# Performance work log

Hardware: AMD Instinct MI355X
Metric: run time of the kernel (lower is better)

Reference implementation:

```python
import jax, jax.numpy as jnp
import numpy as np

B = 256          # batch
T = 256          # block_size (tril mask requires seq_len == 256)
E = 384          # n_embed
H = 6            # n_head
HS = E // H      # head_size = 64
EPS = 1e-5       # torch LayerNorm default


def layernorm(x, g, b):
    m = x.mean(-1, keepdims=True)
    v = x.var(-1, keepdims=True)  # population variance, matches torch LN
    return (x - m) * jax.lax.rsqrt(v + EPS) * g + b


def setup_inputs() -> dict:
    key = jax.random.key(0)
    ks = jax.random.split(key, 8)
    s = lambda i, shape: jax.random.normal(ks[i], shape, jnp.float32) * 0.02
    return {
        "x": jax.random.normal(ks[0], (B, T, E), jnp.float32),
        # per-head Q/K/V linears (bias=False) packed along output dim: [E, H*HS]
        "Wq": s(1, (E, E)), "Wk": s(2, (E, E)), "Wv": s(3, (E, E)),
        "Wo": s(4, (E, E)), "bo": jnp.zeros((E,), jnp.float32),
        "W1": s(5, (E, 4 * E)), "b1": jnp.zeros((4 * E,), jnp.float32),
        "W2": s(6, (4 * E, E)), "b2": jnp.zeros((E,), jnp.float32),
        "g1": jnp.ones((E,), jnp.float32), "be1": jnp.zeros((E,), jnp.float32),
        "g2": jnp.ones((E,), jnp.float32), "be2": jnp.zeros((E,), jnp.float32),
    }


def reference(x, Wq, Wk, Wv, Wo, bo, W1, b1, W2, b2, g1, be1, g2, be2):
    # Block.forward: ffwd(ln2(sa(ln1(x)) + x)) + x   (dropout = identity at eval)
    h = layernorm(x, g1, be1)                                  # [B,T,E]
    q = (h @ Wq).reshape(B, T, H, HS)
    k = (h @ Wk).reshape(B, T, H, HS)
    v = (h @ Wv).reshape(B, T, H, HS)
    wei = jnp.einsum('bqhd,bkhd->bhqk', q, k) * (HS ** -0.5)   # [B,H,T,T]
    mask = jnp.tril(jnp.ones((T, T), dtype=bool))
    wei = jnp.where(mask, wei, -jnp.inf)
    wei = jax.nn.softmax(wei, axis=-1)
    attn = jnp.einsum('bhqk,bkhd->bqhd', wei, v).reshape(B, T, E)
    sa = attn @ Wo + bo                                        # output projection
    y = sa + x                                                 # residual 1
    h2 = layernorm(y, g2, be2)
    ff = jax.nn.relu(h2 @ W1 + b1) @ W2 + b2                   # FFN
    return ff + x                                              # residual 2 (to x!)
```

## Files before the change

### kernel.cpp

```cpp
#include <hip/hip_runtime.h>
#include <hip/hip_bf16.h>

typedef unsigned short bfu;
typedef __attribute__((ext_vector_type(8))) short short8;
typedef __attribute__((ext_vector_type(4))) float f32x4;

__device__ __forceinline__ bfu f2bf(float f) {
  return __builtin_bit_cast(bfu, __float2bfloat16(f));
}

__device__ __forceinline__ void gld16(const void* g, void* l) {
  __builtin_amdgcn_global_load_lds(
      (const __attribute__((address_space(1))) void*)g,
      (__attribute__((address_space(3))) void*)l, 16, 0, 0);
}

__device__ __forceinline__ int swz(int row, int slot) {
  const int unit = row >> 1;
  const int s8 = ((row & 1) << 2) | slot;
  return (unit << 7) + (((s8 ^ unit) & 7) << 4) + ((s8 >> 3) << 7);
}
__device__ __forceinline__ void unswz(int p, int& row, int& colel) {
  const int unit = p >> 7;
  const int s8 = ((p >> 4) & 7) ^ (unit & 7);
  row = (unit << 1) | (s8 >> 2);
  colel = (s8 & 3) << 3;
}

__global__ void transpose_w(const float* __restrict__ W, bfu* __restrict__ WT,
                            int K, int N) {
  int idx = blockIdx.x * 256 + threadIdx.x;
  if (idx >= K * N) return;
  int k = idx / N, n = idx - k * N;
  WT[(size_t)n * K + k] = f2bf(W[idx]);
}

__launch_bounds__(256)
__global__ void ln_kernel(const float* __restrict__ in, const float* __restrict__ g,
                          const float* __restrict__ be, bfu* __restrict__ out) {
  const int wv = threadIdx.x >> 6, ln = threadIdx.x & 63;
  const size_t row = (size_t)blockIdx.x * 4 + wv;
  const float* p = in + row * 384;
  float v[6], s = 0.f, ss = 0.f;
#pragma unroll
  for (int i = 0; i < 6; i++) { v[i] = p[i * 64 + ln]; s += v[i]; ss += v[i] * v[i]; }
#pragma unroll
  for (int m = 1; m < 64; m <<= 1) { s += __shfl_xor(s, m); ss += __shfl_xor(ss, m); }
  const float mean = s * (1.f / 384.f);
  const float rs = rsqrtf(ss * (1.f / 384.f) - mean * mean + 1e-5f);
  bfu* q = out + row * 384;
#pragma unroll
  for (int i = 0; i < 6; i++) {
    const int c = i * 64 + ln;
    q[c] = f2bf((v[i] - mean) * rs * g[c] + be[c]);
  }
}

template <int BIAS, int RELU, int OUTBF>
__launch_bounds__(256)
__global__ void gemm_kernel(const bfu* __restrict__ A, const bfu* __restrict__ Bt,
                            const float* __restrict__ bias,
                            void* __restrict__ Cout, int N, int K, int ntn) {
  __shared__ bfu a_sm[3][128 * 32];
  __shared__ bfu b_sm[3][128 * 32];
  const int tid = threadIdx.x;
  const int wv = tid >> 6, ln = tid & 63;
  const int cpx = gridDim.x >> 3;
  const int wg = (blockIdx.x & 7) * cpx + (blockIdx.x >> 3);
  const int bm = wg / ntn, bn = wg - bm * ntn;
  const int m0 = bm << 7, n0 = bn << 7;
  const int wr = wv >> 1, wc = wv & 1;
  const int fr = ln & 15, fslot = ln >> 4;

  f32x4 acc[4][4];
#pragma unroll
  for (int i = 0; i < 4; i++)
#pragma unroll
    for (int j = 0; j < 4; j++) acc[i][j] = f32x4{0.f, 0.f, 0.f, 0.f};

  auto stage = [&](int buf, int kt) {
#pragma unroll
    for (int i = 0; i < 2; ++i) {
      const int c = wv * 2 + i;
      const int p = c * 1024 + (ln << 4);
      int r, colel;
      unswz(p, r, colel);
      const int col = kt * 32 + colel;
      gld16(A  + (size_t)(m0 + r) * K + col, (char*)a_sm[buf] + c * 1024);
      gld16(Bt + (size_t)(n0 + r) * K + col, (char*)b_sm[buf] + c * 1024);
    }
  };

  const int nk = K >> 5;
  stage(0, 0);
  if (nk > 1) stage(1, 1);

  int cb = 0;
  for (int kt = 0; kt < nk; ++kt) {
    if (kt + 1 < nk) asm volatile("s_waitcnt vmcnt(4)" ::: "memory");
    else             asm volatile("s_waitcnt vmcnt(0)" ::: "memory");
    __builtin_amdgcn_s_barrier();
    __builtin_amdgcn_sched_barrier(0);
    if (kt + 2 < nk) {
      int sb = cb + 2; if (sb >= 3) sb -= 3;
      stage(sb, kt + 2);
    }
    short8 af[4], bfr[4];
#pragma unroll
    for (int mi = 0; mi < 4; mi++)
      af[mi] = *(const short8*)((const char*)a_sm[cb] + swz(wr * 64 + mi * 16 + fr, fslot));
#pragma unroll
    for (int ni = 0; ni < 4; ni++)
      bfr[ni] = *(const short8*)((const char*)b_sm[cb] + swz(wc * 64 + ni * 16 + fr, fslot));
#pragma unroll
    for (int mi = 0; mi < 4; mi++)
#pragma unroll
      for (int ni = 0; ni < 4; ni++)
        acc[mi][ni] = __builtin_amdgcn_mfma_f32_16x16x32_bf16(af[mi], bfr[ni], acc[mi][ni], 0, 0, 0);
    cb = (cb + 1 == 3) ? 0 : cb + 1;
  }

#pragma unroll
  for (int mi = 0; mi < 4; mi++) {
#pragma unroll
    for (int ni = 0; ni < 4; ni++) {
      const int row = m0 + wr * 64 + mi * 16 + ((ln >> 4) << 2);
      const int col = n0 + wc * 64 + ni * 16 + fr;
      float bv = 0.f;
      if (BIAS) bv = bias[col];
#pragma unroll
      for (int r = 0; r < 4; r++) {
        float v = acc[mi][ni][r] + bv;
        if (RELU) v = fmaxf(v, 0.f);
        const size_t idx = (size_t)(row + r) * N + col;
        if (OUTBF) ((bfu*)Cout)[idx] = f2bf(v);
        else       ((float*)Cout)[idx] = v;
      }
    }
  }
}

template <int LN>
__launch_bounds__(512)
__global__ void row_gemm(const bfu* __restrict__ A, const bfu* __restrict__ Bt,
                         const float* __restrict__ bias, const float* __restrict__ res,
                         const float* __restrict__ g, const float* __restrict__ be,
                         void* __restrict__ Cout, int K) {
  __shared__ bfu a_sm[4][128 * 32];
  __shared__ bfu b_sm[4][384 * 32];
  __shared__ float lnp[4][128][2];
  const int tid = threadIdx.x;
  const int wv = tid >> 6, ln = tid & 63;
  const int wr = wv >> 2, wc = wv & 3;
  const int fr = ln & 15, fslot = ln >> 4;
  const int m0 = blockIdx.x << 7;

  f32x4 acc[4][6];
#pragma unroll
  for (int i = 0; i < 4; i++)
#pragma unroll
    for (int j = 0; j < 6; j++) acc[i][j] = f32x4{0.f, 0.f, 0.f, 0.f};

  auto stage = [&](int buf, int kt) {
#pragma unroll
    for (int i = 0; i < 4; ++i) {
      const int c = wv * 4 + i;
      const int cc = (c < 8) ? c : (c - 8);
      const int p = cc * 1024 + (ln << 4);
      int r, colel;
      unswz(p, r, colel);
      const int col = kt * 32 + colel;
      if (c < 8)
        gld16(A + (size_t)(m0 + r) * K + col, (char*)a_sm[buf] + cc * 1024);
      else
        gld16(Bt + (size_t)r * K + col, (char*)b_sm[buf] + cc * 1024);
    }
  };

  const int nk = K >> 5;
#pragma unroll
  for (int i = 0; i < 3; ++i)
    if (i < nk) stage(i, i);

  for (int kt = 0; kt < nk; ++kt) {
    const int rem = nk - 1 - kt;
    if (rem >= 2)      asm volatile("s_waitcnt vmcnt(8)" ::: "memory");
    else if (rem == 1) asm volatile("s_waitcnt vmcnt(4)" ::: "memory");
    else               asm volatile("s_waitcnt vmcnt(0)" ::: "memory");
    __builtin_amdgcn_s_barrier();
    __builtin_amdgcn_sched_barrier(0);
    if (kt + 3 < nk) stage((kt + 3) & 3, kt + 3);
    const int cb = kt & 3;
    short8 af[4], bfr[6];
#pragma unroll
    for (int mi = 0; mi < 4; mi++)
      af[mi] = *(const short8*)((const char*)a_sm[cb] + swz(wr * 64 + mi * 16 + fr, fslot));
#pragma unroll
    for (int ni = 0; ni < 6; ni++)
      bfr[ni] = *(const short8*)((const char*)b_sm[cb] + swz(wc * 96 + ni * 16 + fr, fslot));
#pragma unroll
    for (int mi = 0; mi < 4; mi++)
#pragma unroll
      for (int ni = 0; ni < 6; ni++)
        acc[mi][ni] = __builtin_amdgcn_mfma_f32_16x16x32_bf16(af[mi], bfr[ni], acc[mi][ni], 0, 0, 0);
  }

  const int rq = (ln >> 4) << 2;
#pragma unroll
  for (int mi = 0; mi < 4; mi++) {
    const int row = wr * 64 + mi * 16 + rq;
#pragma unroll
    for (int ni = 0; ni < 6; ni++) {
      const int col = wc * 96 + ni * 16 + fr;
      const float bv = bias[col];
#pragma unroll
      for (int r = 0; r < 4; r++)
        acc[mi][ni][r] += bv + res[(size_t)(m0 + row + r) * 384 + col];
    }
  }

  if (LN) {
#pragma unroll
    for (int mi = 0; mi < 4; mi++) {
      float s[4] = {0.f, 0.f, 0.f, 0.f}, ss[4] = {0.f, 0.f, 0.f, 0.f};
#pragma unroll
      for (int ni = 0; ni < 6; ni++)
#pragma unroll
        for (int r = 0; r < 4; r++) {
          const float v = acc[mi][ni][r];
          s[r] += v; ss[r] += v * v;
        }
#pragma unroll
      for (int m = 1; m < 16; m <<= 1)
#pragma unroll
        for (int r = 0; r < 4; r++) {
          s[r] += __shfl_xor(s[r], m);
          ss[r] += __shfl_xor(ss[r], m);
        }
      if (fr == 0) {
#pragma unroll
        for (int r = 0; r < 4; r++) {
          lnp[wc][wr * 64 + mi * 16 + rq + r][0] = s[r];
          lnp[wc][wr * 64 + mi * 16 + rq + r][1] = ss[r];
        }
      }
    }
    __syncthreads();
#pragma unroll
    for (int mi = 0; mi < 4; mi++) {
#pragma unroll
      for (int r = 0; r < 4; r++) {
        const int row = wr * 64 + mi * 16 + rq + r;
        const float sm = lnp[0][row][0] + lnp[1][row][0] + lnp[2][row][0] + lnp[3][row][0];
        const float sq = lnp[0][row][1] + lnp[1][row][1] + lnp[2][row][1] + lnp[3][row][1];
        const float mean = sm * (1.f / 384.f);
        const float rs = rsqrtf(sq * (1.f / 384.f) - mean * mean + 1e-5f);
#pragma unroll
        for (int ni = 0; ni < 6; ni++) {
          const int col = wc * 96 + ni * 16 + fr;
          ((bfu*)Cout)[(size_t)(m0 + row) * 384 + col] =
              f2bf((acc[mi][ni][r] - mean) * rs * g[col] + be[col]);
        }
      }
    }
  } else {
#pragma unroll
    for (int mi = 0; mi < 4; mi++) {
      const int row = wr * 64 + mi * 16 + rq;
#pragma unroll
      for (int ni = 0; ni < 6; ni++) {
        const int col = wc * 96 + ni * 16 + fr;
#pragma unroll
        for (int r = 0; r < 4; r++)
          ((float*)Cout)[(size_t)(m0 + row + r) * 384 + col] = acc[mi][ni][r];
      }
    }
  }
}

#define KPAD 72
#define VPAD 264
#define PPAD 264

__launch_bounds__(512)
__global__ void attn_kernel(const bfu* __restrict__ qkv, bfu* __restrict__ ob) {
  __shared__ bfu k_sm[256 * KPAD];
  __shared__ bfu vt_sm[64 * VPAD];
  __shared__ bfu p_sm[8 * 16 * PPAD];
  const int b = blockIdx.x / 6, h = blockIdx.x - b * 6;
  const int tid = threadIdx.x;
  const int wv = tid >> 6, ln = tid & 63;
  const int fr = ln & 15, fc = (ln >> 4) << 3;
  const size_t inbase = (size_t)b * 256 * 1152 + h * 64;
  const bfu* qb = qkv + inbase;
  const bfu* kb = qkv + inbase + 384;
  const bfu* vb = qkv + inbase + 768;
  const size_t obase = (size_t)b * 256 * 384 + h * 64;

  {
    const int row = tid >> 1;
    const int dh = (tid & 1) << 5;
    const bfu* kg = kb + (size_t)row * 1152 + dh;
    const bfu* vg = vb + (size_t)row * 1152 + dh;
#pragma unroll
    for (int i = 0; i < 4; i++) {
      short8 t8 = *(const short8*)(kg + i * 8);
      *(short8*)&k_sm[row * KPAD + dh + i * 8] = t8;
      short8 v8 = *(const short8*)(vg + i * 8);
#pragma unroll
      for (int j = 0; j < 8; j++)
        vt_sm[(dh + i * 8 + j) * VPAD + row] = (bfu)v8[j];
    }
  }
  __syncthreads();

  bfu* pw = &p_sm[wv * 16 * PPAD];
  const int rq = (ln >> 4) << 2;

#pragma unroll
  for (int si = 0; si < 2; ++si) {
    const int s = si ? (15 - wv) : wv;
    const int qr0 = s << 4;
    const int nf = s + 1;
    short8 aq[2];
#pragma unroll
    for (int dc = 0; dc < 2; dc++)
      aq[dc] = *(const short8*)(qb + (size_t)(qr0 + fr) * 1152 + dc * 32 + fc);

    f32x4 sacc[16];
#pragma unroll
    for (int f = 0; f < 16; f++) sacc[f] = f32x4{0.f, 0.f, 0.f, 0.f};
#pragma unroll
    for (int f = 0; f < 16; f++) if (f < nf) {
#pragma unroll
      for (int dc = 0; dc < 2; dc++) {
        short8 kf = *(const short8*)&k_sm[(f * 16 + fr) * KPAD + dc * 32 + fc];
        sacc[f] = __builtin_amdgcn_mfma_f32_16x16x32_bf16(aq[dc], kf, sacc[f], 0, 0, 0);
      }
    }
    float mr[4] = {-3e38f, -3e38f, -3e38f, -3e38f};
#pragma unroll
    for (int f = 0; f < 16; f++) if (f < nf) {
#pragma unroll
      for (int r = 0; r < 4; r++) {
        float sv = sacc[f][r] * 0.125f;
        if (f * 16 + fr > qr0 + rq + r) sv = -3e38f;
        sacc[f][r] = sv;
        mr[r] = fmaxf(mr[r], sv);
      }
    }
#pragma unroll
    for (int msk = 1; msk < 16; msk <<= 1) {
#pragma unroll
      for (int r = 0; r < 4; r++) mr[r] = fmaxf(mr[r], __shfl_xor(mr[r], msk));
    }
    float ls[4] = {0.f, 0.f, 0.f, 0.f};
#pragma unroll
    for (int f = 0; f < 16; f++) if (f < nf) {
#pragma unroll
      for (int r = 0; r < 4; r++) {
        float p = __expf(sacc[f][r] - mr[r]);
        sacc[f][r] = p;
        ls[r] += p;
      }
    }
#pragma unroll
    for (int msk = 1; msk < 16; msk <<= 1) {
#pragma unroll
      for (int r = 0; r < 4; r++) ls[r] += __shfl_xor(ls[r], msk);
    }
#pragma unroll
    for (int f = 0; f < 16; f++) if (f < nf) {
#pragma unroll
      for (int r = 0; r < 4; r++)
        pw[(rq + r) * PPAD + f * 16 + fr] = f2bf(sacc[f][r]);
    }
    if (nf & 1) {
#pragma unroll
      for (int r = 0; r < 4; r++) pw[(rq + r) * PPAD + nf * 16 + fr] = 0;
    }
    f32x4 oc[4];
#pragma unroll
    for (int n = 0; n < 4; n++) oc[n] = f32x4{0.f, 0.f, 0.f, 0.f};
    const int kcs = (nf + 1) >> 1;
#pragma unroll
    for (int kc = 0; kc < 8; ++kc) if (kc < kcs) {
      short8 pa = *(const short8*)&pw[fr * PPAD + kc * 32 + fc];
#pragma unroll
      for (int n = 0; n < 4; n++) {
        short8 vf = *(const short8*)&vt_sm[(n * 16 + fr) * VPAD + kc * 32 + fc];
        oc[n] = __builtin_amdgcn_mfma_f32_16x16x32_bf16(pa, vf, oc[n], 0, 0, 0);
      }
    }
    float inv[4];
#pragma unroll
    for (int r = 0; r < 4; r++) inv[r] = 1.f / ls[r];
#pragma unroll
    for (int n = 0; n < 4; n++) {
#pragma unroll
      for (int r = 0; r < 4; r++)
        ob[obase + (size_t)(qr0 + rq + r) * 384 + n * 16 + fr] = f2bf(oc[n][r] * inv[r]);
    }
  }
}

extern "C" void kernel_launch(void* const* d_in, const int* in_sizes, int n_in,
                              void* d_out, int out_size, void* d_ws, size_t ws_size,
                              hipStream_t stream) {
  const float* x   = (const float*)d_in[0];
  const float* Wq  = (const float*)d_in[1];
  const float* Wk  = (const float*)d_in[2];
  const float* Wv  = (const float*)d_in[3];
  const float* Wo  = (const float*)d_in[4];
  const float* bo  = (const float*)d_in[5];
  const float* W1  = (const float*)d_in[6];
  const float* b1  = (const float*)d_in[7];
  const float* W2  = (const float*)d_in[8];
  const float* b2  = (const float*)d_in[9];
  const float* g1  = (const float*)d_in[10];
  const float* be1 = (const float*)d_in[11];
  const float* g2  = (const float*)d_in[12];
  const float* be2 = (const float*)d_in[13];
  float* out = (float*)d_out;
  char* ws = (char*)d_ws;

  bfu* wqkvT = (bfu*)(ws + 0);
  bfu* woT   = (bfu*)(ws + 884736);
  bfu* w1T   = (bfu*)(ws + 1179648);
  bfu* w2T   = (bfu*)(ws + 2359296);
  char* H    = ws + 3538944;
  char* BIG  = H + 50331648;
  bfu* hb    = (bfu*)BIG;
  bfu* qkvb  = (bfu*)(BIG + 50331648);
  bfu* attnb = (bfu*)BIG;
  bfu* h2b   = (bfu*)H;
  bfu* ab    = (bfu*)BIG;

  transpose_w<<<576, 256, 0, stream>>>(Wq, wqkvT, 384, 384);
  transpose_w<<<576, 256, 0, stream>>>(Wk, wqkvT + 384 * 384, 384, 384);
  transpose_w<<<576, 256, 0, stream>>>(Wv, wqkvT + 2 * 384 * 384, 384, 384);
  transpose_w<<<576, 256, 0, stream>>>(Wo, woT, 384, 384);
  transpose_w<<<2304, 256, 0, stream>>>(W1, w1T, 384, 1536);
  transpose_w<<<2304, 256, 0, stream>>>(W2, w2T, 1536, 384);

  ln_kernel<<<16384, 256, 0, stream>>>(x, g1, be1, hb);

  gemm_kernel<0, 0, 1><<<4608, 256, 0, stream>>>(hb, wqkvT, nullptr, qkvb, 1152, 384, 9);

  attn_kernel<<<1536, 512, 0, stream>>>(qkvb, attnb);

  row_gemm<1><<<512, 512, 0, stream>>>(attnb, woT, bo, x, g2, be2, h2b, 384);

  gemm_kernel<1, 1, 1><<<6144, 256, 0, stream>>>(h2b, w1T, b1, ab, 1536, 384, 12);

  row_gemm<0><<<512, 512, 0, stream>>>(ab, w2T, b2, x, nullptr, nullptr, out, 1536);
}
```

Measured before the change: 522.1 us.

## Replace GEMM with 8-wave 256x128 BK=64 pipelined kernel and fuse weight transposes

Introduces gemm8p, an 8-wave kernel with 256x128 tiles and K=64 stages in triple-buffered LDS, using a new row-XOR swizzle, split half-K MFMA phases, barriers and s_setprio around MFMA bursts. It is used for the QKV, FFN1 and FFN2 GEMMs, with FFN2 now adding the residual in a plain epilogue instead of row_gemm. The six weight transpose launches are merged into one kernel, and setprio is added to row_gemm. The aims are more operand reuse per tile, fewer barriers per K step and fewer launches, at the cost of much larger LDS use (about 144KB) that limits occupancy.

```diff
diff --git a/kernel.cpp b/kernel.cpp
--- a/kernel.cpp
+++ b/kernel.cpp
@@ -13,6 +13,10 @@
   __builtin_amdgcn_global_load_lds(
       (const __attribute__((address_space(1))) void*)g,
       (__attribute__((address_space(3))) void*)l, 16, 0, 0);
+}
+
+__device__ __forceinline__ int swz8(int row, int sl) {
+  return (row << 7) + (((sl ^ (row & 7)) & 7) << 4);
 }
 
 __device__ __forceinline__ int swz(int row, int slot) {
@@ -27,12 +31,27 @@
   colel = (s8 & 3) << 3;
 }
 
-__global__ void transpose_w(const float* __restrict__ W, bfu* __restrict__ WT,
-                            int K, int N) {
+__global__ void transpose_all(const float* __restrict__ Wq, const float* __restrict__ Wk,
+                              const float* __restrict__ Wv, const float* __restrict__ Wo,
+                              const float* __restrict__ W1, const float* __restrict__ W2,
+                              bfu* __restrict__ wqkvT, bfu* __restrict__ woT,
+                              bfu* __restrict__ w1T, bfu* __restrict__ w2T) {
   int idx = blockIdx.x * 256 + threadIdx.x;
-  if (idx >= K * N) return;
-  int k = idx / N, n = idx - k * N;
-  WT[(size_t)n * K + k] = f2bf(W[idx]);
+  if (idx < 4 * 147456) {
+    int r = idx / 147456, i = idx - r * 147456;
+    int k = i / 384, n = i - k * 384;
+    const float* W = r == 0 ? Wq : r == 1 ? Wk : r == 2 ? Wv : Wo;
+    bfu* dst = r < 3 ? wqkvT + r * 147456 : woT;
+    dst[n * 384 + k] = f2bf(W[i]);
+  } else if (idx < 4 * 147456 + 589824) {
+    int i = idx - 4 * 147456;
+    int k = i / 1536, n = i - k * 1536;
+    w1T[n * 384 + k] = f2bf(W1[i]);
+  } else if (idx < 4 * 147456 + 2 * 589824) {
+    int i = idx - 4 * 147456 - 589824;
+    int k = i / 384, n = i - k * 384;
+    w2T[(size_t)n * 1536 + k] = f2bf(W2[i]);
+  }
 }
 
 __launch_bounds__(256)
@@ -56,19 +75,18 @@
   }
 }
 
-template <int BIAS, int RELU, int OUTBF>
-__launch_bounds__(256)
-__global__ void gemm_kernel(const bfu* __restrict__ A, const bfu* __restrict__ Bt,
-                            const float* __restrict__ bias,
-                            void* __restrict__ Cout, int N, int K, int ntn) {
-  __shared__ bfu a_sm[3][128 * 32];
-  __shared__ bfu b_sm[3][128 * 32];
+template <int BIAS, int RELU, int RES, int OUTBF>
+__launch_bounds__(512)
+__global__ void gemm8p(const bfu* __restrict__ A, const bfu* __restrict__ Bt,
+                       const float* __restrict__ bias, const float* __restrict__ res,
+                       void* __restrict__ Cout, int N, int K, int ntn) {
+  __shared__ bfu sm[3][384 * 64];
   const int tid = threadIdx.x;
   const int wv = tid >> 6, ln = tid & 63;
   const int cpx = gridDim.x >> 3;
   const int wg = (blockIdx.x & 7) * cpx + (blockIdx.x >> 3);
   const int bm = wg / ntn, bn = wg - bm * ntn;
-  const int m0 = bm << 7, n0 = bn << 7;
+  const int m0 = bm << 8, n0 = bn << 7;
   const int wr = wv >> 1, wc = wv & 1;
   const int fr = ln & 15, fslot = ln >> 4;
 
@@ -78,53 +96,85 @@
 #pragma unroll
     for (int j = 0; j < 4; j++) acc[i][j] = f32x4{0.f, 0.f, 0.f, 0.f};
 
-  auto stage = [&](int buf, int kt) {
+  const int lr = ln >> 3;
+  const int lslot = (ln & 7) ^ lr;
+
+  auto stage = [&](int s, int kt) {
+    char* smA = (char*)sm[s];
+    char* smB = smA + 256 * 64 * 2;
+    const int kcol = (kt << 6) + (lslot << 3);
+#pragma unroll
+    for (int i = 0; i < 4; ++i) {
+      const int c = (wv << 2) + i;
+      gld16(A + (size_t)(m0 + (c << 3) + lr) * K + kcol, smA + (c << 10));
+    }
 #pragma unroll
     for (int i = 0; i < 2; ++i) {
-      const int c = wv * 2 + i;
-      const int p = c * 1024 + (ln << 4);
-      int r, colel;
-      unswz(p, r, colel);
-      const int col = kt * 32 + colel;
-      gld16(A  + (size_t)(m0 + r) * K + col, (char*)a_sm[buf] + c * 1024);
-      gld16(Bt + (size_t)(n0 + r) * K + col, (char*)b_sm[buf] + c * 1024);
+      const int c = (wv << 1) + i;
+      gld16(Bt + (size_t)(n0 + (c << 3) + lr) * K + kcol, smB + (c << 10));
     }
   };
 
-  const int nk = K >> 5;
+  const int nk = K >> 6;
   stage(0, 0);
-  if (nk > 1) stage(1, 1);
-
-  int cb = 0;
+  if (nk > 1) {
+    stage(1, 1);
+    asm volatile("s_waitcnt vmcnt(6)" ::: "memory");
+  } else {
+    asm volatile("s_waitcnt vmcnt(0)" ::: "memory");
+  }
+  __builtin_amdgcn_s_barrier();
+
   for (int kt = 0; kt < nk; ++kt) {
-    if (kt + 1 < nk) asm volatile("s_waitcnt vmcnt(4)" ::: "memory");
-    else             asm volatile("s_waitcnt vmcnt(0)" ::: "memory");
+    const int s = kt - (kt / 3) * 3;
+    const char* smA = (const char*)sm[s];
+    const char* smB = smA + 256 * 64 * 2;
+    if (kt + 2 < nk) stage((kt + 2) - ((kt + 2) / 3) * 3, kt + 2);
+    short8 af[4], bf[4];
+#pragma unroll
+    for (int mi = 0; mi < 4; mi++)
+      af[mi] = *(const short8*)(smA + swz8(wr * 64 + mi * 16 + fr, fslot));
+#pragma unroll
+    for (int ni = 0; ni < 4; ni++)
+      bf[ni] = *(const short8*)(smB + swz8(wc * 64 + ni * 16 + fr, fslot));
     __builtin_amdgcn_s_barrier();
+    asm volatile("s_waitcnt lgkmcnt(0)" ::: "memory");
     __builtin_amdgcn_sched_barrier(0);
-    if (kt + 2 < nk) {
-      int sb = cb + 2; if (sb >= 3) sb -= 3;
-      stage(sb, kt + 2);
-    }
-    short8 af[4], bfr[4];
+    __builtin_amdgcn_s_setprio(1);
 #pragma unroll
     for (int mi = 0; mi < 4; mi++)
-      af[mi] = *(const short8*)((const char*)a_sm[cb] + swz(wr * 64 + mi * 16 + fr, fslot));
+#pragma unroll
+      for (int ni = 0; ni < 4; ni++)
+        acc[mi][ni] = __builtin_amdgcn_mfma_f32_16x16x32_bf16(af[mi], bf[ni], acc[mi][ni], 0, 0, 0);
+    __builtin_amdgcn_s_setprio(0);
+    __builtin_amdgcn_s_barrier();
+#pragma unroll
+    for (int mi = 0; mi < 4; mi++)
+      af[mi] = *(const short8*)(smA + swz8(wr * 64 + mi * 16 + fr, 4 + fslot));
 #pragma unroll
     for (int ni = 0; ni < 4; ni++)
-      bfr[ni] = *(const short8*)((const char*)b_sm[cb] + swz(wc * 64 + ni * 16 + fr, fslot));
+      bf[ni] = *(const short8*)(smB + swz8(wc * 64 + ni * 16 + fr, 4 + fslot));
+    __builtin_amdgcn_s_barrier();
+    asm volatile("s_waitcnt lgkmcnt(0)" ::: "memory");
+    __builtin_amdgcn_sched_barrier(0);
+    __builtin_amdgcn_s_setprio(1);
 #pragma unroll
     for (int mi = 0; mi < 4; mi++)
 #pragma unroll
       for (int ni = 0; ni < 4; ni++)
-        acc[mi][ni] = __builtin_amdgcn_mfma_f32_16x16x32_bf16(af[mi], bfr[ni], acc[mi][ni], 0, 0, 0);
-    cb = (cb + 1 == 3) ? 0 : cb + 1;
-  }
-
+        acc[mi][ni] = __builtin_amdgcn_mfma_f32_16x16x32_bf16(af[mi], bf[ni], acc[mi][ni], 0, 0, 0);
+    __builtin_amdgcn_s_setprio(0);
+    if (kt + 2 < nk)      asm volatile("s_waitcnt vmcnt(6)" ::: "memory");
+    else if (kt + 1 < nk) asm volatile("s_waitcnt vmcnt(0)" ::: "memory");
+    __builtin_amdgcn_s_barrier();
+  }
+
+  const int rq = (ln >> 4) << 2;
 #pragma unroll
   for (int mi = 0; mi < 4; mi++) {
 #pragma unroll
     for (int ni = 0; ni < 4; ni++) {
-      const int row = m0 + wr * 64 + mi * 16 + ((ln >> 4) << 2);
+      const int row = m0 + wr * 64 + mi * 16 + rq;
       const int col = n0 + wc * 64 + ni * 16 + fr;
       float bv = 0.f;
       if (BIAS) bv = bias[col];
@@ -133,6 +183,7 @@
         float v = acc[mi][ni][r] + bv;
         if (RELU) v = fmaxf(v, 0.f);
         const size_t idx = (size_t)(row + r) * N + col;
+        if (RES) v += res[idx];
         if (OUTBF) ((bfu*)Cout)[idx] = f2bf(v);
         else       ((float*)Cout)[idx] = v;
       }
@@ -198,11 +249,13 @@
 #pragma unroll
     for (int ni = 0; ni < 6; ni++)
       bfr[ni] = *(const short8*)((const char*)b_sm[cb] + swz(wc * 96 + ni * 16 + fr, fslot));
+    __builtin_amdgcn_s_setprio(1);
 #pragma unroll
     for (int mi = 0; mi < 4; mi++)
 #pragma unroll
       for (int ni = 0; ni < 6; ni++)
         acc[mi][ni] = __builtin_amdgcn_mfma_f32_16x16x32_bf16(af[mi], bfr[ni], acc[mi][ni], 0, 0, 0);
+    __builtin_amdgcn_s_setprio(0);
   }
 
   const int rq = (ln >> 4) << 2;
@@ -436,22 +489,17 @@
   bfu* h2b   = (bfu*)H;
   bfu* ab    = (bfu*)BIG;
 
-  transpose_w<<<576, 256, 0, stream>>>(Wq, wqkvT, 384, 384);
-  transpose_w<<<576, 256, 0, stream>>>(Wk, wqkvT + 384 * 384, 384, 384);
-  transpose_w<<<576, 256, 0, stream>>>(Wv, wqkvT + 2 * 384 * 384, 384, 384);
-  transpose_w<<<576, 256, 0, stream>>>(Wo, woT, 384, 384);
-  transpose_w<<<2304, 256, 0, stream>>>(W1, w1T, 384, 1536);
-  transpose_w<<<2304, 256, 0, stream>>>(W2, w2T, 1536, 384);
+  transpose_all<<<6912, 256, 0, stream>>>(Wq, Wk, Wv, Wo, W1, W2, wqkvT, woT, w1T, w2T);
 
   ln_kernel<<<16384, 256, 0, stream>>>(x, g1, be1, hb);
 
-  gemm_kernel<0, 0, 1><<<4608, 256, 0, stream>>>(hb, wqkvT, nullptr, qkvb, 1152, 384, 9);
+  gemm8p<0, 0, 0, 1><<<2304, 512, 0, stream>>>(hb, wqkvT, nullptr, nullptr, qkvb, 1152, 384, 9);
 
   attn_kernel<<<1536, 512, 0, stream>>>(qkvb, attnb);
 
   row_gemm<1><<<512, 512, 0, stream>>>(attnb, woT, bo, x, g2, be2, h2b, 384);
 
-  gemm_kernel<1, 1, 1><<<6144, 256, 0, stream>>>(h2b, w1T, b1, ab, 1536, 384, 12);
-
-  row_gemm<0><<<512, 512, 0, stream>>>(ab, w2T, b2, x, nullptr, nullptr, out, 1536);
-}
+  gemm8p<1, 1, 0, 1><<<3072, 512, 0, stream>>>(h2b, w1T, b1, nullptr, ab, 1536, 384, 12);
+
+  gemm8p<1, 0, 1, 0><<<768, 512, 0, stream>>>(ab, w2T, b2, x, out, 384, 1536, 3);
+}
```

After: 509.6 us. 1.02x faster.
